# Kernel tuning notes

Measured on AMD Instinct MI355X. Metric: run time of the kernel, lower is better.

## Reference

```python
import jax, jax.numpy as jnp
import numpy as np

_K = 256  # d_model // 8


def setup_inputs() -> dict:
    key = jax.random.key(0)
    ks = jax.random.split(key, 7)
    B, T, D = 4, 4096, 2048
    x = jax.random.normal(ks[0], (B, T, D), jnp.float32)
    ema_mean = 0.1 * jax.random.normal(ks[1], (D,), jnp.float32)
    # ensure positive variance: ema_sq - ema_mean^2 in [0.5, 1.5]
    ema_sq = ema_mean ** 2 + 0.5 + jax.random.uniform(ks[2], (D,), jnp.float32)
    ema_out = jax.random.normal(ks[3], (D,), jnp.float32)
    log_tau = 0.1 * jax.random.normal(ks[4], (), jnp.float32)
    log_sigma_raw = 0.1 * jax.random.normal(ks[5], (), jnp.float32)
    log_w_raw = 0.1 * jax.random.normal(ks[6], (), jnp.float32)
    return {
        "x": x,
        "ema_mean": ema_mean,
        "ema_sq": ema_sq,
        "ema_out": ema_out,
        "log_tau": log_tau,
        "log_sigma_raw": log_sigma_raw,
        "log_w_raw": log_w_raw,
    }


def reference(x, ema_mean, ema_sq, ema_out, log_tau, log_sigma_raw, log_w_raw):
    tau = jnp.exp(log_tau)
    sigma = jax.nn.softplus(log_sigma_raw) + 0.01
    w = jax.nn.softplus(log_w_raw)

    out = jax.nn.gelu(x, approximate=False)  # F.gelu default = exact erf

    # z-score against EMA stats
    std = jnp.sqrt(jnp.clip(ema_sq - ema_mean ** 2, 1e-6, None))
    z = (x - ema_mean) / std

    # topk |z| over channel dim, gather z, mean of |z_topk|
    _, idx = jax.lax.top_k(jnp.abs(z), _K)          # idx: [B,T,K]
    z_topk = jnp.take_along_axis(z, idx, axis=-1)
    topk_mean = jnp.mean(jnp.abs(z_topk), axis=-1, keepdims=True)  # [B,T,1]
    surp = jnp.tanh(sigma * topk_mean)

    # cosine similarity of gelu output against EMA output direction
    ema_u = ema_out / (jnp.linalg.norm(ema_out) + 1e-8)
    out_n = out / jnp.maximum(
        jnp.linalg.norm(out, axis=-1, keepdims=True), 1e-12
    )  # F.normalize eps
    cos_out = jnp.sum(out_n * ema_u, axis=-1, keepdims=True)  # [B,T,1]

    gate = jnp.exp(-tau * cos_out) * (1.0 + w * surp)
    return out * gate
```

## Files before the change

### kernel.cpp

```cpp
#include <hip/hip_runtime.h>
#include <math.h>

#define D      2048
#define KSEL   256
#define NT     256
#define NBINS  512
#define ROWS   2

typedef float f4 __attribute__((ext_vector_type(4)));
typedef int   i4 __attribute__((ext_vector_type(4)));

__device__ __forceinline__ float fast_gelu(float x) {
    float x2 = x * x;
    float t  = fmaf(x2, -0.0713548162f, -1.5957691216f);
    float e  = __expf(x * t);
    return x * __builtin_amdgcn_rcpf(1.0f + e);
}

template<int CTRL, int RMASK>
__device__ __forceinline__ float dpp_mov_f(float v) {
    int r = __builtin_amdgcn_update_dpp(0, __builtin_bit_cast(int, v),
                                        CTRL, RMASK, 0xf, true);
    return __builtin_bit_cast(float, r);
}
template<int CTRL, int RMASK>
__device__ __forceinline__ int dpp_mov_i(int v) {
    return __builtin_amdgcn_update_dpp(0, v, CTRL, RMASK, 0xf, true);
}
__device__ __forceinline__ float wave_scan_f(float x) {
    x += dpp_mov_f<0x111, 0xf>(x);
    x += dpp_mov_f<0x112, 0xf>(x);
    x += dpp_mov_f<0x114, 0xf>(x);
    x += dpp_mov_f<0x118, 0xf>(x);
    x += dpp_mov_f<0x142, 0xa>(x);
    x += dpp_mov_f<0x143, 0xc>(x);
    return x;
}
__device__ __forceinline__ int wave_scan_i(int x) {
    x += dpp_mov_i<0x111, 0xf>(x);
    x += dpp_mov_i<0x112, 0xf>(x);
    x += dpp_mov_i<0x114, 0xf>(x);
    x += dpp_mov_i<0x118, 0xf>(x);
    x += dpp_mov_i<0x142, 0xa>(x);
    x += dpp_mov_i<0x143, 0xc>(x);
    return x;
}
__device__ __forceinline__ float wave_bcast63_f(float x) {
    int r = __builtin_amdgcn_readlane(__builtin_bit_cast(int, x), 63);
    return __builtin_bit_cast(float, r);
}

__global__ __launch_bounds__(NT) void row_kernel(
    const float* __restrict__ x,
    const float* __restrict__ ema_mean,
    const float* __restrict__ ema_sq,
    const float* __restrict__ ema_out,
    const float* __restrict__ p_log_tau,
    const float* __restrict__ p_log_sigma,
    const float* __restrict__ p_log_w,
    float* __restrict__ out)
{
    __shared__ int   hist[ROWS][NBINS];
    __shared__ float ssred[4];
    __shared__ float red[ROWS][4][2];
    __shared__ float gate_sh[ROWS];

    const int t    = threadIdx.x;
    const int wave = t >> 6;
    const int lane = t & 63;

    const float tau   = __expf(p_log_tau[0]);
    const float sigma = __logf(1.0f + __expf(p_log_sigma[0])) + 0.01f;
    const float w     = __logf(1.0f + __expf(p_log_w[0]));

    f4 m0 = ((const f4*)ema_mean)[t];
    f4 m1 = ((const f4*)ema_mean)[t + NT];
    f4 q0 = ((const f4*)ema_sq)[t];
    f4 q1 = ((const f4*)ema_sq)[t + NT];
    f4 e0 = ((const f4*)ema_out)[t];
    f4 e1 = ((const f4*)ema_out)[t + NT];

    const float mv[8] = {m0.x,m0.y,m0.z,m0.w, m1.x,m1.y,m1.z,m1.w};
    const float qv[8] = {q0.x,q0.y,q0.z,q0.w, q1.x,q1.y,q1.z,q1.w};
    const float ev[8] = {e0.x,e0.y,e0.z,e0.w, e1.x,e1.y,e1.z,e1.w};

    float a_[8], b_[8];
    float ss = 0.f;
#pragma unroll
    for (int j = 0; j < 8; ++j) {
        float v = fmaxf(fmaf(-mv[j], mv[j], qv[j]), 1e-6f);
        a_[j] = 64.0f * __builtin_amdgcn_rsqf(v);
        b_[j] = -mv[j] * a_[j];
        ss = fmaf(ev[j], ev[j], ss);
    }
    ss = wave_scan_f(ss);
    if (lane == 63) ssred[wave] = ss;

    const size_t row0 = (size_t)blockIdx.x * ROWS;
    f4 xa = ((const f4*)(x + row0 * D))[t];
    f4 xb = ((const f4*)(x + row0 * D))[t + NT];

    hist[0][t] = 0;  hist[0][t + NT] = 0;
    hist[1][t] = 0;  hist[1][t + NT] = 0;
    __syncthreads();

    const float inv_nrm =
        1.0f / (sqrtf(ssred[0] + ssred[1] + ssred[2] + ssred[3]) + 1e-8f);
    float u_[8];
#pragma unroll
    for (int j = 0; j < 8; ++j) u_[j] = ev[j] * inv_nrm;

#pragma unroll
    for (int r = 0; r < ROWS; ++r) {
        const float xv[8] = {xa.x,xa.y,xa.z,xa.w, xb.x,xb.y,xb.z,xb.w};

        float g[8], av[8];
        float dot = 0.f, nrm = 0.f;
#pragma unroll
        for (int j = 0; j < 8; ++j) {
            float gg = fast_gelu(xv[j]);
            g[j] = gg;
            av[j] = fabsf(fmaf(xv[j], a_[j], b_[j]));
            dot = fmaf(gg, u_[j], dot);
            nrm = fmaf(gg, gg, nrm);
        }

        if (r + 1 < ROWS) {
            const float* xn = x + (row0 + r + 1) * D;
            xa = ((const f4*)xn)[t];
            xb = ((const f4*)xn)[t + NT];
        }

        dot = wave_scan_f(dot);
        nrm = wave_scan_f(nrm);
        if (lane == 63) { red[r][wave][0] = dot; red[r][wave][1] = nrm; }

#pragma unroll
        for (int j = 0; j < 8; ++j) {
            int bin = (int)av[j];
            bin = bin > NBINS - 1 ? NBINS - 1 : bin;
            atomicAdd(&hist[r][(NBINS - 1) - bin], 1);
        }
        __syncthreads();

        if (wave == 0) {
            i4 va = *(const i4*)&hist[r][8 * lane];
            i4 vb = *(const i4*)&hist[r][8 * lane + 4];
            const float base = 511.5f - (float)(8 * lane);
            int c0 = va.x;
            int c1 = c0 + va.y;
            int c2 = c1 + va.z;
            int c3 = c2 + va.w;
            int c4 = c3 + vb.x;
            int c5 = c4 + vb.y;
            int c6 = c5 + vb.z;
            int c7 = c6 + vb.w;
            float w0 = (float)va.x * base;
            float w1 = fmaf((float)va.y, base - 1.0f, w0);
            float w2 = fmaf((float)va.z, base - 2.0f, w1);
            float w3 = fmaf((float)va.w, base - 3.0f, w2);
            float w4 = fmaf((float)vb.x, base - 4.0f, w3);
            float w5 = fmaf((float)vb.y, base - 5.0f, w4);
            float w6 = fmaf((float)vb.z, base - 6.0f, w5);
            float w7 = fmaf((float)vb.w, base - 7.0f, w6);

            int   incl  = wave_scan_i(c7);
            int   excl  = incl - c7;
            float winc  = wave_scan_f(w7);
            float wexcl = winc - w7;

            float ts = 0.f;
            {
                const int   pre[8]  = {0, c0, c1, c2, c3, c4, c5, c6};
                const int   cum[8]  = {c0, c1, c2, c3, c4, c5, c6, c7};
                const float wpre[8] = {0.f, w0, w1, w2, w3, w4, w5, w6};
#pragma unroll
                for (int k = 0; k < 8; ++k) {
                    int s0  = excl + pre[k];
                    int e0x = excl + cum[k];
                    if (s0 < KSEL && e0x >= KSEL)
                        ts = fmaf((float)(KSEL - s0), base - (float)k,
                                  wexcl + wpre[k]);
                }
            }
            ts = wave_bcast63_f(wave_scan_f(ts));

            float dd = red[r][0][0] + red[r][1][0] + red[r][2][0] + red[r][3][0];
            float nn = red[r][0][1] + red[r][1][1] + red[r][2][1] + red[r][3][1];

            const float topk_mean = ts * (1.0f / (64.0f * KSEL));
            const float cosv = dd * __builtin_amdgcn_rsqf(fmaxf(nn, 1e-24f));
            const float yt = sigma * topk_mean;
            const float et = __expf(-2.0f * yt);
            const float th = (1.0f - et) * __builtin_amdgcn_rcpf(1.0f + et);
            const float gate = __expf(-tau * cosv) * fmaf(w, th, 1.0f);
            if (lane == 0) gate_sh[r] = gate;
        }
        __syncthreads();

        const float gate = gate_sh[r];
        f4 oa, ob;
        oa.x = g[0]*gate; oa.y = g[1]*gate; oa.z = g[2]*gate; oa.w = g[3]*gate;
        ob.x = g[4]*gate; ob.y = g[5]*gate; ob.z = g[6]*gate; ob.w = g[7]*gate;
        f4* outr = (f4*)(out + (row0 + r) * D);
        outr[t]      = oa;
        outr[t + NT] = ob;
    }
}

extern "C" void kernel_launch(void* const* d_in, const int* in_sizes, int n_in,
                              void* d_out, int out_size, void* d_ws, size_t ws_size,
                              hipStream_t stream) {
    (void)n_in; (void)out_size; (void)d_ws; (void)ws_size;
    const float* x         = (const float*)d_in[0];
    const float* ema_mean  = (const float*)d_in[1];
    const float* ema_sq    = (const float*)d_in[2];
    const float* ema_out   = (const float*)d_in[3];
    const float* log_tau   = (const float*)d_in[4];
    const float* log_sigma = (const float*)d_in[5];
    const float* log_w     = (const float*)d_in[6];
    float* out = (float*)d_out;

    const int rows = in_sizes[0] / D;
    row_kernel<<<rows / ROWS, NT, 0, stream>>>(x, ema_mean, ema_sq, ema_out,
                                               log_tau, log_sigma, log_w, out);
}
```

Measured before the change: 45.14 us.

## Process eight rows per block with double-buffered histograms and earlier prefetch

Each block now handles eight rows instead of two, so there are four times fewer blocks and the per-block setup (EMA loads, norm reduction) is amortized. The histogram and reduction buffers become two ping-pong slots. While wave 0 computes the gate, idle waves zero the other slot, which removes a separate clearing pass per row. The next row's loads are issued at the top of each iteration so they overlap the GELU and reduction work, and launch bounds ask for higher occupancy. The trade-off is fewer blocks in flight and a serial chain of per-row barriers inside each block, which could reduce memory-level parallelism.

```diff
diff --git a/kernel.cpp b/kernel.cpp
--- a/kernel.cpp
+++ b/kernel.cpp
@@ -5,7 +5,7 @@
 #define KSEL   256
 #define NT     256
 #define NBINS  512
-#define ROWS   2
+#define ROWS   8
 
 typedef float f4 __attribute__((ext_vector_type(4)));
 typedef int   i4 __attribute__((ext_vector_type(4)));
@@ -50,7 +50,7 @@
     return __builtin_bit_cast(float, r);
 }
 
-__global__ __launch_bounds__(NT) void row_kernel(
+__global__ __launch_bounds__(NT, 8) void row_kernel(
     const float* __restrict__ x,
     const float* __restrict__ ema_mean,
     const float* __restrict__ ema_sq,
@@ -60,10 +60,10 @@
     const float* __restrict__ p_log_w,
     float* __restrict__ out)
 {
-    __shared__ int   hist[ROWS][NBINS];
+    __shared__ int   hist[2][NBINS];
     __shared__ float ssred[4];
-    __shared__ float red[ROWS][4][2];
-    __shared__ float gate_sh[ROWS];
+    __shared__ float red[2][4][2];
+    __shared__ float gate_sh[2];
 
     const int t    = threadIdx.x;
     const int wave = t >> 6;
@@ -110,10 +110,17 @@
 #pragma unroll
     for (int j = 0; j < 8; ++j) u_[j] = ev[j] * inv_nrm;
 
-#pragma unroll
     for (int r = 0; r < ROWS; ++r) {
+        const int p = r & 1;
+
+        f4 nxa, nxb;
+        if (r + 1 < ROWS) {
+            const float* xn = x + (row0 + r + 1) * D;
+            nxa = ((const f4*)xn)[t];
+            nxb = ((const f4*)xn)[t + NT];
+        }
+
         const float xv[8] = {xa.x,xa.y,xa.z,xa.w, xb.x,xb.y,xb.z,xb.w};
-
         float g[8], av[8];
         float dot = 0.f, nrm = 0.f;
 #pragma unroll
@@ -125,27 +132,21 @@
             nrm = fmaf(gg, gg, nrm);
         }
 
-        if (r + 1 < ROWS) {
-            const float* xn = x + (row0 + r + 1) * D;
-            xa = ((const f4*)xn)[t];
-            xb = ((const f4*)xn)[t + NT];
-        }
-
         dot = wave_scan_f(dot);
         nrm = wave_scan_f(nrm);
-        if (lane == 63) { red[r][wave][0] = dot; red[r][wave][1] = nrm; }
+        if (lane == 63) { red[p][wave][0] = dot; red[p][wave][1] = nrm; }
 
 #pragma unroll
         for (int j = 0; j < 8; ++j) {
             int bin = (int)av[j];
             bin = bin > NBINS - 1 ? NBINS - 1 : bin;
-            atomicAdd(&hist[r][(NBINS - 1) - bin], 1);
+            atomicAdd(&hist[p][(NBINS - 1) - bin], 1);
         }
         __syncthreads();
 
         if (wave == 0) {
-            i4 va = *(const i4*)&hist[r][8 * lane];
-            i4 vb = *(const i4*)&hist[r][8 * lane + 4];
+            i4 va = *(const i4*)&hist[p][8 * lane];
+            i4 vb = *(const i4*)&hist[p][8 * lane + 4];
             const float base = 511.5f - (float)(8 * lane);
             int c0 = va.x;
             int c1 = c0 + va.y;
@@ -185,8 +186,8 @@
             }
             ts = wave_bcast63_f(wave_scan_f(ts));
 
-            float dd = red[r][0][0] + red[r][1][0] + red[r][2][0] + red[r][3][0];
-            float nn = red[r][0][1] + red[r][1][1] + red[r][2][1] + red[r][3][1];
+            float dd = red[p][0][0] + red[p][1][0] + red[p][2][0] + red[p][3][0];
+            float nn = red[p][0][1] + red[p][1][1] + red[p][2][1] + red[p][3][1];
 
             const float topk_mean = ts * (1.0f / (64.0f * KSEL));
             const float cosv = dd * __builtin_amdgcn_rsqf(fmaxf(nn, 1e-24f));
@@ -194,17 +195,24 @@
             const float et = __expf(-2.0f * yt);
             const float th = (1.0f - et) * __builtin_amdgcn_rcpf(1.0f + et);
             const float gate = __expf(-tau * cosv) * fmaf(w, th, 1.0f);
-            if (lane == 0) gate_sh[r] = gate;
+            if (lane == 0) gate_sh[p] = gate;
+        } else {
+            if (t - 64 < NBINS / 4) {
+                i4 z = (i4)0;
+                ((i4*)&hist[p ^ 1][0])[t - 64] = z;
+            }
         }
         __syncthreads();
 
-        const float gate = gate_sh[r];
+        const float gate = gate_sh[p];
         f4 oa, ob;
         oa.x = g[0]*gate; oa.y = g[1]*gate; oa.z = g[2]*gate; oa.w = g[3]*gate;
         ob.x = g[4]*gate; ob.y = g[5]*gate; ob.z = g[6]*gate; ob.w = g[7]*gate;
         f4* outr = (f4*)(out + (row0 + r) * D);
         outr[t]      = oa;
         outr[t + NT] = ob;
+
+        xa = nxa; xb = nxb;
     }
 }
 
```

Result: slower. 93.08 us (+106.2%).
